# Kernel optimization log

Hardware: AMD Instinct MI355X
Metric: run time of the kernel (lower is better)

## Reference

```python
import jax, jax.numpy as jnp
import numpy as np

N, C, SI, VI, H, R = 10000, 2, 128, 16, 4, 32
SH, VH = SI // H, VI // H  # 32, 4
EPS = 1e-8

def _vnorm(x, axis):
    # clamped L2 norm, matches _norm_no_nan
    return jnp.sqrt(jnp.clip(jnp.sum(x * x, axis=axis), EPS, None))

def _gvp_full(s, v, wh, ws_w, ws_b, wv, wsv_w, wsv_b):
    # GVP with activations=(silu, sigmoid), vector_gate=True, vi=vo
    vh = jnp.swapaxes(v, -1, -2) @ wh            # [..., 3, h]
    vn = _vnorm(vh, -2)                          # [..., h]
    so = jnp.concatenate([s, vn], -1) @ ws_w + ws_b
    vo = jnp.swapaxes(vh @ wv, -1, -2)           # [..., vo, 3]
    gate = jax.nn.sigmoid(jax.nn.sigmoid(so) @ wsv_w + wsv_b)
    return jax.nn.silu(so), vo * gate[..., None]

def setup_inputs():
    key = jax.random.key(0)
    ks = iter(jax.random.split(key, 40))
    def lin(i, o):
        return jax.random.normal(next(ks), (i, o), jnp.float32) / np.sqrt(i)
    def bias(o):
        return 0.02 * jax.random.normal(next(ks), (o,), jnp.float32)
    inp = {}
    inp['s'] = jax.random.normal(next(ks), (N, C, SI), jnp.float32)
    inp['v'] = jax.random.normal(next(ks), (N, C, VI, 3), jnp.float32)
    # weight_proj: GVP((SI,VI)->(R,0)), no activations; h_dim = max(VI,0) = VI
    inp['wp_wh'] = lin(VI, VI); inp['wp_ws_w'] = lin(VI + SI, R); inp['wp_ws_b'] = bias(R)
    # to_q/k/v: GVP((SI,VI)->(SI,VI)), silu/sigmoid, vector_gate; h_dim = VI
    for p in ('q', 'k', 'vv'):
        inp[p + '_wh'] = lin(VI, VI)
        inp[p + '_ws_w'] = lin(VI + SI, SI); inp[p + '_ws_b'] = bias(SI)
        inp[p + '_wv'] = lin(VI, VI)
        inp[p + '_wsv_w'] = lin(SI, VI); inp[p + '_wsv_b'] = bias(VI)
    # attn_gvp_long: GVP((2*SH, 2*VH) -> (1,0)), no activations; h_dim = 2*VH
    inp['attn_wh'] = lin(2 * VH, 2 * VH)
    inp['attn_ws_w'] = lin(2 * VH + 2 * SH, 1); inp['attn_ws_b'] = bias(1)
    return inp

def reference(s, v, wp_wh, wp_ws_w, wp_ws_b,
              q_wh, q_ws_w, q_ws_b, q_wv, q_wsv_w, q_wsv_b,
              k_wh, k_ws_w, k_ws_b, k_wv, k_wsv_w, k_wsv_b,
              vv_wh, vv_ws_w, vv_ws_b, vv_wv, vv_wsv_w, vv_wsv_b,
              attn_wh, attn_ws_w, attn_ws_b):
    n, c = s.shape[:2]
    # ---- Compress: softmax-pool N -> R anchors ----
    vh = jnp.swapaxes(v, -1, -2) @ wp_wh          # [N,C,3,VI]
    vn = _vnorm(vh, -2)                            # [N,C,VI]
    pw = jnp.concatenate([s, vn], -1) @ wp_ws_w + wp_ws_b  # [N,C,R]
    pw = jax.nn.softmax(pw, axis=0)                # softmax over nodes
    s_g = jnp.einsum('nca,ncs->acs', pw, s)        # [R,C,SI] (includes transpose(0,1))
    v_g = jnp.einsum('nca,ncvd->acvd', pw, v)      # [R,C,VI,3]
    # ---- q from nodes, k/v from anchors ----
    qs, qv = _gvp_full(s, v, q_wh, q_ws_w, q_ws_b, q_wv, q_wsv_w, q_wsv_b)
    ks, kv = _gvp_full(s_g, v_g, k_wh, k_ws_w, k_ws_b, k_wv, k_wsv_w, k_wsv_b)
    vs, vv_ = _gvp_full(s_g, v_g, vv_wh, vv_ws_w, vv_ws_b, vv_wv, vv_wsv_w, vv_wsv_b)
    qs = qs.reshape(n, c, H, SH); qv = qv.reshape(n, c, H, VH, 3)
    ks = ks.reshape(R, c, H, SH); kv = kv.reshape(R, c, H, VH, 3)
    vs = vs.reshape(R, c, H, SH); vv_ = vv_.reshape(R, c, H, VH, 3)
    # ---- attention GVP on cat(q, k): split weights instead of materializing concat ----
    wh_q, wh_k = attn_wh[:VH], attn_wh[VH:]        # wh @ cat(qv,kv) = qv@wh_q + kv@wh_k
    qh = jnp.swapaxes(qv, -1, -2) @ wh_q           # [N,C,H,3,2VH]
    kh = jnp.swapaxes(kv, -1, -2) @ wh_k           # [R,C,H,3,2VH]
    vn2 = _vnorm(qh[:, None] + kh[None], -2)       # [N,R,C,H,2VH]
    ws_q = attn_ws_w[:SH]; ws_k = attn_ws_w[SH:2 * SH]; ws_n = attn_ws_w[2 * SH:]
    e = (qs @ ws_q)[:, None] + (ks @ ws_k)[None] + vn2 @ ws_n + attn_ws_b  # [N,R,C,H,1]
    e = e[..., 0] / np.sqrt(SH)
    alpha = jax.nn.softmax(e, axis=1)              # softmax over anchors (dim=1)
    # ---- Broadcast: weighted sum of anchor values ----
    out_s = jnp.einsum('nrch,rchd->nchd', alpha, vs).reshape(n, c, SI)
    out_v = jnp.einsum('nrch,rchde->nchde', alpha, vv_).reshape(n, c, VI, 3)
    return out_s, out_v
```

## Files before the change

kernel.cpp:

```cpp
#include <hip/hip_runtime.h>
#include <hip/hip_bf16.h>


#define N_  10000
#define C_  2
#define SI_ 128
#define VI_ 16
#define H_  4
#define R_  32
#define SH_ 32
#define VH_ 4
#define NC_ (N_*C_)

#define ROWS_ 16
#define XSTR_ 20

typedef const float* __restrict__ fptr;

__device__ __forceinline__ float sigm(float x){ return 1.f/(1.f+__expf(-x)); }

#define OFF_LG   0
#define OFF_EQH  640000
#define OFF_SG   2640000
#define OFF_TKH  2651520
#define OFF_TEK  2657664
#define OFF_TVS  2657920
#define OFF_TVV  2666112

#define SGSTRIDE_ 180

__global__ __launch_bounds__(256) void kA(
    fptr s, fptr v,
    fptr wp_wh, fptr wp_ws_w, fptr wp_ws_b,
    fptr q_wh, fptr q_ws_w, fptr q_ws_b, fptr q_wv, fptr q_wsv_w, fptr q_wsv_b,
    fptr attn_wh, fptr attn_ws_w,
    float* __restrict__ pexp, float* __restrict__ eqh,
    float* __restrict__ sgz)
{
  __shared__ __align__(16) float ARENA[160*XSTR_];
  __shared__ __align__(16) float VVs[ROWS_*48];
  __shared__ __align__(16) float VHQ[ROWS_*48];
  __shared__ __align__(16) float SO[ROWS_*128];
  __shared__ __align__(16) float GATE[ROWS_*16];
  __shared__ __align__(16) float QV[ROWS_*48];
  float* const XT  = ARENA;
  float* const SIG = ARENA;

  const int tid  = threadIdx.x;
  const int row0 = blockIdx.x * ROWS_;

  if (blockIdx.x == 0){
    for (int i = tid; i < 64*SGSTRIDE_; i += 256) sgz[i] = 0.f;
  }

  for (int idx = tid; idx < ROWS_*128; idx += 256){
    int r = idx >> 7, j = idx & 127;
    XT[j*XSTR_ + r] = s[(row0+r)*128 + j];
  }
  for (int idx = tid; idx < ROWS_*48; idx += 256){
    int r = idx / 48, k = idx - r*48;
    VVs[r*48 + k] = v[(row0+r)*48 + k];
  }
  __syncthreads();

  for (int idx = tid; idx < ROWS_*32; idx += 256){
    int r = idx >> 5, ii = idx & 31, path = ii >> 4, i = ii & 15;
    fptr wh = path ? wp_wh : q_wh;
    float h0=0.f, h1=0.f, h2=0.f;
    #pragma unroll
    for (int j = 0; j < 16; j++){
      float w = wh[j*16 + i];
      h0 = fmaf(VVs[r*48 + j*3 + 0], w, h0);
      h1 = fmaf(VVs[r*48 + j*3 + 1], w, h1);
      h2 = fmaf(VVs[r*48 + j*3 + 2], w, h2);
    }
    float vn = sqrtf(fmaxf(h0*h0 + h1*h1 + h2*h2, 1e-8f));
    if (!path){
      VHQ[r*48 +  0 + i] = h0;
      VHQ[r*48 + 16 + i] = h1;
      VHQ[r*48 + 32 + i] = h2;
      XT[(128+i)*XSTR_ + r] = vn;
    } else {
      XT[(144+i)*XSTR_ + r] = vn;
    }
  }
  __syncthreads();

  const int colA = tid & 127, rgA = tid >> 7;
  float acc[8];
  {
    float bqs = q_ws_b[colA];
    #pragma unroll
    for (int k = 0; k < 8; k++) acc[k] = bqs;
    const float* xbA = &XT[rgA*8];
    #pragma unroll 8
    for (int j = 0; j < 144; j++){
      float w = q_ws_w[j*128 + colA];
      const float* xb = xbA + j*XSTR_;
      float4 x0 = *(const float4*)(xb + 0);
      float4 x1 = *(const float4*)(xb + 4);
      acc[0] = fmaf(x0.x, w, acc[0]); acc[1] = fmaf(x0.y, w, acc[1]);
      acc[2] = fmaf(x0.z, w, acc[2]); acc[3] = fmaf(x0.w, w, acc[3]);
      acc[4] = fmaf(x1.x, w, acc[4]); acc[5] = fmaf(x1.y, w, acc[5]);
      acc[6] = fmaf(x1.z, w, acc[6]); acc[7] = fmaf(x1.w, w, acc[7]);
    }
  }
  {
    const int colB = tid & 31, rgB = tid >> 5;
    float b0 = wp_ws_b[colB];
    float a0 = b0, a1 = b0;
    #pragma unroll 8
    for (int j = 0; j < 144; j++){
      int jj = (j < 128) ? j : (j + 16);
      float w = wp_ws_w[j*32 + colB];
      const float* xb = &XT[jj*XSTR_ + rgB*2];
      a0 = fmaf(xb[0], w, a0);
      a1 = fmaf(xb[1], w, a1);
    }
    const int n = (row0 >> 1) + rgB;
    pexp[(0*32 + colB)*N_ + n] = __expf(a0);
    pexp[(1*32 + colB)*N_ + n] = __expf(a1);
  }
  __syncthreads();

  #pragma unroll
  for (int k = 0; k < 8; k++){
    float so = acc[k];
    float sg_ = sigm(so);
    SIG[(rgA*8 + k)*128 + colA] = sg_;
    SO [(rgA*8 + k)*128 + colA] = so * sg_;
  }
  __syncthreads();

  {
    const int r = tid >> 4, g = tid & 15;
    float ga = q_wsv_b[g];
    #pragma unroll 8
    for (int o = 0; o < 128; o += 4){
      float4 s4 = *(const float4*)&SIG[r*128 + o];
      ga = fmaf(s4.x, q_wsv_w[(o+0)*16 + g], ga);
      ga = fmaf(s4.y, q_wsv_w[(o+1)*16 + g], ga);
      ga = fmaf(s4.z, q_wsv_w[(o+2)*16 + g], ga);
      ga = fmaf(s4.w, q_wsv_w[(o+3)*16 + g], ga);
    }
    GATE[r*16 + g] = sigm(ga);
  }
  __syncthreads();

  for (int t = tid; t < 64 + ROWS_*48; t += 256){
    if (t < 64){
      const int r = t >> 2, h = t & 3;
      float e = 0.f;
      #pragma unroll
      for (int u = 0; u < 32; u++)
        e = fmaf(SO[r*128 + h*32 + u], attn_ws_w[u], e);
      eqh[(row0 + r)*100 + h] = e;
    } else {
      const int t2 = t - 64;
      int r = t2 / 48, k = t2 - r*48, i = k / 3, d = k - i*3;
      float a = 0.f;
      #pragma unroll
      for (int j = 0; j < 16; j++)
        a = fmaf(VHQ[r*48 + d*16 + j], q_wv[j*16 + i], a);
      QV[r*48 + k] = a * GATE[r*16 + i];
    }
  }
  __syncthreads();

  for (int t = tid; t < ROWS_*96; t += 256){
    int r = t / 96, k = t - r*96;
    int h = k / 24, rem = k - h*24, d = rem >> 3, ee = rem & 7;
    float a = 0.f;
    #pragma unroll
    for (int i = 0; i < 4; i++)
      a = fmaf(QV[r*48 + (h*4 + i)*3 + d], attn_wh[i*8 + ee], a);
    eqh[(row0 + r)*100 + 8 + k] = a;
  }
}

__global__ __launch_bounds__(256) void kAccum(const float* __restrict__ pexp,
                                              fptr s, fptr v,
                                              float* __restrict__ sg)
{
  const int b = blockIdx.x;
  const int c = b & 1, ah = (b >> 1) & 1, chunk = b >> 2;
  const int n0 = chunk * 50;
  const int tid = threadIdx.x;
  const int ag = tid >> 6, dl = tid & 63;
  const int abase = ah*16 + ag*4;

  const float* pb = pexp + (c*32 + abase)*N_;
  float acc[4][3] = {};
  float dn[4] = {};

  #pragma unroll 2
  for (int n = n0; n < n0 + 50; n++){
    const int rc = n*2 + c;
    float pw[4];
    #pragma unroll
    for (int aa = 0; aa < 4; aa++){
      pw[aa] = pb[aa*N_ + n];
      dn[aa] += pw[aa];
    }
    #pragma unroll
    for (int dd = 0; dd < 3; dd++){
      int d = dl + 64*dd;
      if (d < 176){
        float xv = (d < 128) ? s[rc*128 + d] : v[rc*48 + d - 128];
        #pragma unroll
        for (int aa = 0; aa < 4; aa++)
          acc[aa][dd] = fmaf(pw[aa], xv, acc[aa][dd]);
      }
    }
  }
  #pragma unroll
  for (int aa = 0; aa < 4; aa++){
    const int base = (c*32 + abase + aa)*SGSTRIDE_;
    #pragma unroll
    for (int dd = 0; dd < 3; dd++){
      int d = dl + 64*dd;
      if (d < 176) atomicAdd(&sg[base + d], acc[aa][dd]);
    }
    if (dl == 0) atomicAdd(&sg[base + 176], dn[aa]);
  }
}

__global__ __launch_bounds__(256) void kSmall(
    const float* __restrict__ sg,
    fptr k_wh, fptr k_ws_w, fptr k_ws_b, fptr k_wv, fptr k_wsv_w, fptr k_wsv_b,
    fptr vv_wh, fptr vv_ws_w, fptr vv_ws_b, fptr vv_wv, fptr vv_wsv_w, fptr vv_wsv_b,
    fptr attn_wh, fptr attn_ws_w,
    float* __restrict__ tkh, float* __restrict__ tek,
    float* __restrict__ tvs, float* __restrict__ tvv)
{
  const int b = blockIdx.x, r = b >> 1, c = b & 1;
  const int tid = threadIdx.x;
  __shared__ float X[176];
  __shared__ float VN[2][16];
  __shared__ float VH[2][48];
  __shared__ float SOk[128], SOv[128];
  __shared__ float G[2][16];
  __shared__ float KV[48];

  if (tid < 176){
    const float* p = sg + (c*32 + r)*SGSTRIDE_;
    X[tid] = p[tid] / p[176];
  }
  __syncthreads();

  if (tid < 32){
    int path = tid >> 4, i = tid & 15;
    fptr wh = path ? vv_wh : k_wh;
    float h0=0.f, h1=0.f, h2=0.f;
    #pragma unroll
    for (int j = 0; j < 16; j++){
      float w = wh[j*16 + i];
      h0 = fmaf(X[128 + j*3 + 0], w, h0);
      h1 = fmaf(X[128 + j*3 + 1], w, h1);
      h2 = fmaf(X[128 + j*3 + 2], w, h2);
    }
    VH[path][ 0 + i] = h0; VH[path][16 + i] = h1; VH[path][32 + i] = h2;
    VN[path][i] = sqrtf(fmaxf(h0*h0 + h1*h1 + h2*h2, 1e-8f));
  }
  __syncthreads();

  {
    int path = tid >> 7, col = tid & 127;
    fptr W  = path ? vv_ws_w : k_ws_w;
    fptr Bb = path ? vv_ws_b : k_ws_b;
    float so = Bb[col];
    for (int j = 0; j < 128; j++) so = fmaf(X[j], W[j*128 + col], so);
    #pragma unroll
    for (int i = 0; i < 16; i++)  so = fmaf(VN[path][i], W[(128+i)*128 + col], so);
    (path ? SOv : SOk)[col] = so;
  }
  __syncthreads();

  if (tid < 32){
    int path = tid >> 4, g = tid & 15;
    fptr Wsv = path ? vv_wsv_w : k_wsv_w;
    fptr Bsv = path ? vv_wsv_b : k_wsv_b;
    const float* SOp = path ? SOv : SOk;
    float ga = Bsv[g];
    for (int o = 0; o < 128; o++)
      ga = fmaf(sigm(SOp[o]), Wsv[o*16 + g], ga);
    G[path][g] = sigm(ga);
  } else if (tid < 36){
    int h = tid - 32;
    float e = 0.f;
    #pragma unroll
    for (int t = 0; t < 32; t++){
      float so = SOk[h*32 + t];
      e = fmaf(so * sigm(so), attn_ws_w[32 + t], e);
    }
    tek[(r*2 + c)*4 + h] = e;
  } else if (tid >= 64 && tid < 192){
    int o = tid - 64;
    float so = SOv[o];
    tvs[(r*2 + c)*128 + o] = so * sigm(so);
  }
  __syncthreads();

  if (tid < 96){
    int path = tid / 48, k = tid % 48, i = k / 3, d = k - i*3;
    fptr Wv = path ? vv_wv : k_wv;
    float vo = 0.f;
    #pragma unroll
    for (int j = 0; j < 16; j++)
      vo = fmaf(VH[path][d*16 + j], Wv[j*16 + i], vo);
    float gv = vo * G[path][i];
    if (path == 0) KV[k] = gv;
    else {
      int h = i >> 2, ii = i & 3;
      tvv[(((r*2 + c)*4 + h)*4 + ii)*3 + d] = gv;
    }
  }
  __syncthreads();

  if (tid < 96){
    int h = tid / 24, rem = tid % 24, d = rem >> 3, ee = rem & 7;
    float a = 0.f;
    #pragma unroll
    for (int i = 0; i < 4; i++)
      a = fmaf(KV[(h*4 + i)*3 + d], attn_wh[(4 + i)*8 + ee], a);
    tkh[((r*2 + c)*4 + h)*24 + d*8 + ee] = a;
  }
}

__global__ __launch_bounds__(256) void kAttn(
    const float* __restrict__ eqh,
    const float* __restrict__ tkh, const float* __restrict__ tek,
    const float* __restrict__ tvs, const float* __restrict__ tvv,
    fptr attn_ws_w, fptr attn_ws_b,
    float* __restrict__ out)
{
  __shared__ __align__(16) float KH[64*28];
  __shared__ __align__(16) float VS[64*36];
  __shared__ __align__(16) float VV[64*12];
  __shared__ float EK[64];
  const int tid = threadIdx.x;
  const int h      = blockIdx.x & 3;
  const int rowblk = blockIdx.x >> 2;

  for (int i = tid; i < 64*24; i += 256){
    int m = i / 24, t = i - m*24;
    KH[m*28 + t] = tkh[(m*4 + h)*24 + t];
  }
  for (int i = tid; i < 64*32; i += 256){
    int m = i >> 5, t = i & 31;
    VS[m*36 + t] = tvs[m*128 + h*32 + t];
  }
  for (int i = tid; i < 64*12; i += 256){
    int m = i / 12, t = i - m*12;
    VV[m*12 + t] = tvv[(m*4 + h)*12 + t];
  }
  if (tid < 64) EK[tid] = tek[tid*4 + h];

  float wsn[8];
  #pragma unroll
  for (int ee = 0; ee < 8; ee++) wsn[ee] = attn_ws_w[64 + ee];
  const float wb = attn_ws_b[0];
  __syncthreads();

  const int rh  = tid & 3;
  const int row = rowblk*64 + (tid >> 2);
  if (row < NC_){
    const int c = row & 1;
    const float eq = eqh[row*100 + h];
    float qh[24];
    {
      const float4* qp = (const float4*)&eqh[row*100 + 8 + h*24];
      #pragma unroll
      for (int k = 0; k < 6; k++){
        float4 t4 = qp[k];
        qh[k*4+0] = t4.x; qh[k*4+1] = t4.y; qh[k*4+2] = t4.z; qh[k*4+3] = t4.w;
      }
    }
    float4 accs4[8];
    float4 accv4[3];
    #pragma unroll
    for (int q = 0; q < 8; q++) accs4[q] = make_float4(0.f,0.f,0.f,0.f);
    #pragma unroll
    for (int q = 0; q < 3; q++) accv4[q] = make_float4(0.f,0.f,0.f,0.f);
    float den = 0.f;

    #pragma unroll
    for (int rr = 0; rr < 8; rr++){
      const int m = (rh*8 + rr)*2 + c;
      const float* khp = &KH[m*28];
      float en = 0.f;
      #pragma unroll
      for (int ee = 0; ee < 8; ee++){
        float a0 = qh[ee]      + khp[ee];
        float a1 = qh[8 + ee]  + khp[8 + ee];
        float a2 = qh[16 + ee] + khp[16 + ee];
        en = fmaf(sqrtf(fmaxf(a0*a0 + a1*a1 + a2*a2, 1e-8f)), wsn[ee], en);
      }
      const float w = __expf((eq + EK[m] + en + wb) * 0.17677669529663687f);
      den += w;
      const float4* vp4 = (const float4*)&VS[m*36];
      #pragma unroll
      for (int q = 0; q < 8; q++){
        float4 t4 = vp4[q];
        accs4[q].x = fmaf(w, t4.x, accs4[q].x);
        accs4[q].y = fmaf(w, t4.y, accs4[q].y);
        accs4[q].z = fmaf(w, t4.z, accs4[q].z);
        accs4[q].w = fmaf(w, t4.w, accs4[q].w);
      }
      const float4* vv4 = (const float4*)&VV[m*12];
      #pragma unroll
      for (int q = 0; q < 3; q++){
        float4 t4 = vv4[q];
        accv4[q].x = fmaf(w, t4.x, accv4[q].x);
        accv4[q].y = fmaf(w, t4.y, accv4[q].y);
        accv4[q].z = fmaf(w, t4.z, accv4[q].z);
        accv4[q].w = fmaf(w, t4.w, accv4[q].w);
      }
    }

    #pragma unroll
    for (int q = 0; q < 8; q++){
      accs4[q].x += __shfl_xor(accs4[q].x, 1, 64);
      accs4[q].x += __shfl_xor(accs4[q].x, 2, 64);
      accs4[q].y += __shfl_xor(accs4[q].y, 1, 64);
      accs4[q].y += __shfl_xor(accs4[q].y, 2, 64);
      accs4[q].z += __shfl_xor(accs4[q].z, 1, 64);
      accs4[q].z += __shfl_xor(accs4[q].z, 2, 64);
      accs4[q].w += __shfl_xor(accs4[q].w, 1, 64);
      accs4[q].w += __shfl_xor(accs4[q].w, 2, 64);
    }
    #pragma unroll
    for (int q = 0; q < 3; q++){
      accv4[q].x += __shfl_xor(accv4[q].x, 1, 64);
      accv4[q].x += __shfl_xor(accv4[q].x, 2, 64);
      accv4[q].y += __shfl_xor(accv4[q].y, 1, 64);
      accv4[q].y += __shfl_xor(accv4[q].y, 2, 64);
      accv4[q].z += __shfl_xor(accv4[q].z, 1, 64);
      accv4[q].z += __shfl_xor(accv4[q].z, 2, 64);
      accv4[q].w += __shfl_xor(accv4[q].w, 1, 64);
      accv4[q].w += __shfl_xor(accv4[q].w, 2, 64);
    }
    den += __shfl_xor(den, 1, 64);
    den += __shfl_xor(den, 2, 64);

    if (rh == 0){
      const float inv = 1.f / den;
      float4* po = (float4*)&out[row*128 + h*32];
      #pragma unroll
      for (int q = 0; q < 8; q++){
        float4 t4 = accs4[q];
        t4.x *= inv; t4.y *= inv; t4.z *= inv; t4.w *= inv;
        po[q] = t4;
      }
      float4* pv = (float4*)&out[NC_*128 + row*48 + h*12];
      #pragma unroll
      for (int q = 0; q < 3; q++){
        float4 t4 = accv4[q];
        t4.x *= inv; t4.y *= inv; t4.z *= inv; t4.w *= inv;
        pv[q] = t4;
      }
    }
  }
}

extern "C" void kernel_launch(void* const* d_in, const int* in_sizes, int n_in,
                              void* d_out, int out_size, void* d_ws, size_t ws_size,
                              hipStream_t stream)
{
  fptr s        = (fptr)d_in[0];
  fptr v        = (fptr)d_in[1];
  fptr wp_wh    = (fptr)d_in[2];
  fptr wp_ws_w  = (fptr)d_in[3];
  fptr wp_ws_b  = (fptr)d_in[4];
  fptr q_wh     = (fptr)d_in[5];
  fptr q_ws_w   = (fptr)d_in[6];
  fptr q_ws_b   = (fptr)d_in[7];
  fptr q_wv     = (fptr)d_in[8];
  fptr q_wsv_w  = (fptr)d_in[9];
  fptr q_wsv_b  = (fptr)d_in[10];
  fptr k_wh     = (fptr)d_in[11];
  fptr k_ws_w   = (fptr)d_in[12];
  fptr k_ws_b   = (fptr)d_in[13];
  fptr k_wv     = (fptr)d_in[14];
  fptr k_wsv_w  = (fptr)d_in[15];
  fptr k_wsv_b  = (fptr)d_in[16];
  fptr vv_wh    = (fptr)d_in[17];
  fptr vv_ws_w  = (fptr)d_in[18];
  fptr vv_ws_b  = (fptr)d_in[19];
  fptr vv_wv    = (fptr)d_in[20];
  fptr vv_wsv_w = (fptr)d_in[21];
  fptr vv_wsv_b = (fptr)d_in[22];
  fptr attn_wh  = (fptr)d_in[23];
  fptr attn_ws_w= (fptr)d_in[24];
  fptr attn_ws_b= (fptr)d_in[25];

  float* ws   = (float*)d_ws;
  float* pexp = ws + OFF_LG;
  float* eqh  = ws + OFF_EQH;
  float* sg   = ws + OFF_SG;
  float* tkh  = ws + OFF_TKH;
  float* tek  = ws + OFF_TEK;
  float* tvs  = ws + OFF_TVS;
  float* tvv  = ws + OFF_TVV;

  kA<<<NC_/ROWS_, 256, 0, stream>>>(s, v, wp_wh, wp_ws_w, wp_ws_b,
                                    q_wh, q_ws_w, q_ws_b, q_wv, q_wsv_w, q_wsv_b,
                                    attn_wh, attn_ws_w, pexp, eqh, sg);
  kAccum<<<800, 256, 0, stream>>>(pexp, s, v, sg);
  kSmall<<<64, 256, 0, stream>>>(sg,
                                 k_wh, k_ws_w, k_ws_b, k_wv, k_wsv_w, k_wsv_b,
                                 vv_wh, vv_ws_w, vv_ws_b, vv_wv, vv_wsv_w, vv_wsv_b,
                                 attn_wh, attn_ws_w, tkh, tek, tvs, tvv);
  kAttn<<<((NC_ + 63)/64)*4, 256, 0, stream>>>(eqh, tkh, tek, tvs, tvv,
                                               attn_ws_w, attn_ws_b, (float*)d_out);
}
```

Before: 232.8 us.

## Restructure kA projection GEMM to row-per-lane with fused wp path and attention dot

```diff
diff --git a/kernel.cpp b/kernel.cpp
--- a/kernel.cpp
+++ b/kernel.cpp
@@ -13,7 +13,9 @@
 #define NC_ (N_*C_)
 
 #define ROWS_ 16
-#define XSTR_ 20
+#define XR_   132
+#define VNR_  18
+#define SGR_  129
 
 typedef const float* __restrict__ fptr;
 
@@ -37,14 +39,14 @@
     float* __restrict__ pexp, float* __restrict__ eqh,
     float* __restrict__ sgz)
 {
-  __shared__ __align__(16) float ARENA[160*XSTR_];
+  __shared__ __align__(16) float X[16*XR_];
+  __shared__ float VNQ[16*VNR_];
+  __shared__ float VNP[16*VNR_];
   __shared__ __align__(16) float VVs[ROWS_*48];
   __shared__ __align__(16) float VHQ[ROWS_*48];
-  __shared__ __align__(16) float SO[ROWS_*128];
+  __shared__ float SIG[16*SGR_];
   __shared__ __align__(16) float GATE[ROWS_*16];
   __shared__ __align__(16) float QV[ROWS_*48];
-  float* const XT  = ARENA;
-  float* const SIG = ARENA;
 
   const int tid  = threadIdx.x;
   const int row0 = blockIdx.x * ROWS_;
@@ -55,7 +57,7 @@
 
   for (int idx = tid; idx < ROWS_*128; idx += 256){
     int r = idx >> 7, j = idx & 127;
-    XT[j*XSTR_ + r] = s[(row0+r)*128 + j];
+    X[r*XR_ + j] = s[(row0+r)*128 + j];
   }
   for (int idx = tid; idx < ROWS_*48; idx += 256){
     int r = idx / 48, k = idx - r*48;
@@ -79,102 +81,135 @@
       VHQ[r*48 +  0 + i] = h0;
       VHQ[r*48 + 16 + i] = h1;
       VHQ[r*48 + 32 + i] = h2;
-      XT[(128+i)*XSTR_ + r] = vn;
+      VNQ[r*VNR_ + i] = vn;
     } else {
-      XT[(144+i)*XSTR_ + r] = vn;
-    }
-  }
-  __syncthreads();
-
-  const int colA = tid & 127, rgA = tid >> 7;
+      VNP[r*VNR_ + i] = vn;
+    }
+  }
+  __syncthreads();
+
+  const int r  = tid & 15;
+  const int cg = tid >> 4;
+  const float* xrow = &X[r*XR_];
+  fptr wqb = q_ws_w  + cg*8;
+  fptr wpb = wp_ws_w + cg*2;
+
   float acc[8];
+  #pragma unroll
+  for (int cc = 0; cc < 8; cc++) acc[cc] = q_ws_b[cg*8 + cc];
+  float b2[2];
+  b2[0] = wp_ws_b[cg*2]; b2[1] = wp_ws_b[cg*2 + 1];
+
+  #pragma unroll 2
+  for (int j4 = 0; j4 < 32; j4++){
+    const int j = j4*4;
+    float4 x4 = *(const float4*)(xrow + j);
+    {
+      float4 wa = *(const float4*)(wqb + (j+0)*128);
+      float4 wb = *(const float4*)(wqb + (j+0)*128 + 4);
+      float2 wp = *(const float2*)(wpb + (j+0)*32);
+      acc[0]=fmaf(x4.x,wa.x,acc[0]); acc[1]=fmaf(x4.x,wa.y,acc[1]);
+      acc[2]=fmaf(x4.x,wa.z,acc[2]); acc[3]=fmaf(x4.x,wa.w,acc[3]);
+      acc[4]=fmaf(x4.x,wb.x,acc[4]); acc[5]=fmaf(x4.x,wb.y,acc[5]);
+      acc[6]=fmaf(x4.x,wb.z,acc[6]); acc[7]=fmaf(x4.x,wb.w,acc[7]);
+      b2[0]=fmaf(x4.x,wp.x,b2[0]);   b2[1]=fmaf(x4.x,wp.y,b2[1]);
+    }
+    {
+      float4 wa = *(const float4*)(wqb + (j+1)*128);
+      float4 wb = *(const float4*)(wqb + (j+1)*128 + 4);
+      float2 wp = *(const float2*)(wpb + (j+1)*32);
+      acc[0]=fmaf(x4.y,wa.x,acc[0]); acc[1]=fmaf(x4.y,wa.y,acc[1]);
+      acc[2]=fmaf(x4.y,wa.z,acc[2]); acc[3]=fmaf(x4.y,wa.w,acc[3]);
+      acc[4]=fmaf(x4.y,wb.x,acc[4]); acc[5]=fmaf(x4.y,wb.y,acc[5]);
+      acc[6]=fmaf(x4.y,wb.z,acc[6]); acc[7]=fmaf(x4.y,wb.w,acc[7]);
+      b2[0]=fmaf(x4.y,wp.x,b2[0]);   b2[1]=fmaf(x4.y,wp.y,b2[1]);
+    }
+    {
+      float4 wa = *(const float4*)(wqb + (j+2)*128);
+      float4 wb = *(const float4*)(wqb + (j+2)*128 + 4);
+      float2 wp = *(const float2*)(wpb + (j+2)*32);
+      acc[0]=fmaf(x4.z,wa.x,acc[0]); acc[1]=fmaf(x4.z,wa.y,acc[1]);
+      acc[2]=fmaf(x4.z,wa.z,acc[2]); acc[3]=fmaf(x4.z,wa.w,acc[3]);
+      acc[4]=fmaf(x4.z,wb.x,acc[4]); acc[5]=fmaf(x4.z,wb.y,acc[5]);
+      acc[6]=fmaf(x4.z,wb.z,acc[6]); acc[7]=fmaf(x4.z,wb.w,acc[7]);
+      b2[0]=fmaf(x4.z,wp.x,b2[0]);   b2[1]=fmaf(x4.z,wp.y,b2[1]);
+    }
+    {
+      float4 wa = *(const float4*)(wqb + (j+3)*128);
+      float4 wb = *(const float4*)(wqb + (j+3)*128 + 4);
+      float2 wp = *(const float2*)(wpb + (j+3)*32);
+      acc[0]=fmaf(x4.w,wa.x,acc[0]); acc[1]=fmaf(x4.w,wa.y,acc[1]);
+      acc[2]=fmaf(x4.w,wa.z,acc[2]); acc[3]=fmaf(x4.w,wa.w,acc[3]);
+      acc[4]=fmaf(x4.w,wb.x,acc[4]); acc[5]=fmaf(x4.w,wb.y,acc[5]);
+      acc[6]=fmaf(x4.w,wb.z,acc[6]); acc[7]=fmaf(x4.w,wb.w,acc[7]);
+      b2[0]=fmaf(x4.w,wp.x,b2[0]);   b2[1]=fmaf(x4.w,wp.y,b2[1]);
+    }
+  }
+  #pragma unroll 4
+  for (int i = 0; i < 16; i++){
+    float xq = VNQ[r*VNR_ + i];
+    float4 wa = *(const float4*)(wqb + (128+i)*128);
+    float4 wb = *(const float4*)(wqb + (128+i)*128 + 4);
+    acc[0]=fmaf(xq,wa.x,acc[0]); acc[1]=fmaf(xq,wa.y,acc[1]);
+    acc[2]=fmaf(xq,wa.z,acc[2]); acc[3]=fmaf(xq,wa.w,acc[3]);
+    acc[4]=fmaf(xq,wb.x,acc[4]); acc[5]=fmaf(xq,wb.y,acc[5]);
+    acc[6]=fmaf(xq,wb.z,acc[6]); acc[7]=fmaf(xq,wb.w,acc[7]);
+    float xp = VNP[r*VNR_ + i];
+    float2 wp = *(const float2*)(wpb + (128+i)*32);
+    b2[0]=fmaf(xp,wp.x,b2[0]);   b2[1]=fmaf(xp,wp.y,b2[1]);
+  }
+
   {
-    float bqs = q_ws_b[colA];
-    #pragma unroll
-    for (int k = 0; k < 8; k++) acc[k] = bqs;
-    const float* xbA = &XT[rgA*8];
-    #pragma unroll 8
-    for (int j = 0; j < 144; j++){
-      float w = q_ws_w[j*128 + colA];
-      const float* xb = xbA + j*XSTR_;
-      float4 x0 = *(const float4*)(xb + 0);
-      float4 x1 = *(const float4*)(xb + 4);
-      acc[0] = fmaf(x0.x, w, acc[0]); acc[1] = fmaf(x0.y, w, acc[1]);
-      acc[2] = fmaf(x0.z, w, acc[2]); acc[3] = fmaf(x0.w, w, acc[3]);
-      acc[4] = fmaf(x1.x, w, acc[4]); acc[5] = fmaf(x1.y, w, acc[5]);
-      acc[6] = fmaf(x1.z, w, acc[6]); acc[7] = fmaf(x1.w, w, acc[7]);
-    }
+    float ep = 0.f;
+    const int tq = (cg & 3)*8;
+    #pragma unroll
+    for (int cc = 0; cc < 8; cc++){
+      float so  = acc[cc];
+      float sg_ = sigm(so);
+      SIG[r*SGR_ + cg*8 + cc] = sg_;
+      ep = fmaf(so*sg_, attn_ws_w[tq + cc], ep);
+    }
+    ep += __shfl_xor(ep, 16, 64);
+    ep += __shfl_xor(ep, 32, 64);
+    if ((tid & 63) < 16)
+      eqh[(row0 + r)*100 + (cg >> 2)] = ep;
   }
   {
-    const int colB = tid & 31, rgB = tid >> 5;
-    float b0 = wp_ws_b[colB];
-    float a0 = b0, a1 = b0;
-    #pragma unroll 8
-    for (int j = 0; j < 144; j++){
-      int jj = (j < 128) ? j : (j + 16);
-      float w = wp_ws_w[j*32 + colB];
-      const float* xb = &XT[jj*XSTR_ + rgB*2];
-      a0 = fmaf(xb[0], w, a0);
-      a1 = fmaf(xb[1], w, a1);
-    }
-    const int n = (row0 >> 1) + rgB;
-    pexp[(0*32 + colB)*N_ + n] = __expf(a0);
-    pexp[(1*32 + colB)*N_ + n] = __expf(a1);
-  }
-  __syncthreads();
-
-  #pragma unroll
-  for (int k = 0; k < 8; k++){
-    float so = acc[k];
-    float sg_ = sigm(so);
-    SIG[(rgA*8 + k)*128 + colA] = sg_;
-    SO [(rgA*8 + k)*128 + colA] = so * sg_;
+    const int gr = row0 + r, c = gr & 1, n = gr >> 1;
+    pexp[(c*32 + cg*2    )*N_ + n] = __expf(b2[0]);
+    pexp[(c*32 + cg*2 + 1)*N_ + n] = __expf(b2[1]);
   }
   __syncthreads();
 
   {
-    const int r = tid >> 4, g = tid & 15;
+    const int rr = tid >> 4, g = tid & 15;
+    const float* sp = &SIG[rr*SGR_];
     float ga = q_wsv_b[g];
     #pragma unroll 8
-    for (int o = 0; o < 128; o += 4){
-      float4 s4 = *(const float4*)&SIG[r*128 + o];
-      ga = fmaf(s4.x, q_wsv_w[(o+0)*16 + g], ga);
-      ga = fmaf(s4.y, q_wsv_w[(o+1)*16 + g], ga);
-      ga = fmaf(s4.z, q_wsv_w[(o+2)*16 + g], ga);
-      ga = fmaf(s4.w, q_wsv_w[(o+3)*16 + g], ga);
-    }
-    GATE[r*16 + g] = sigm(ga);
-  }
-  __syncthreads();
-
-  for (int t = tid; t < 64 + ROWS_*48; t += 256){
-    if (t < 64){
-      const int r = t >> 2, h = t & 3;
-      float e = 0.f;
-      #pragma unroll
-      for (int u = 0; u < 32; u++)
-        e = fmaf(SO[r*128 + h*32 + u], attn_ws_w[u], e);
-      eqh[(row0 + r)*100 + h] = e;
-    } else {
-      const int t2 = t - 64;
-      int r = t2 / 48, k = t2 - r*48, i = k / 3, d = k - i*3;
-      float a = 0.f;
-      #pragma unroll
-      for (int j = 0; j < 16; j++)
-        a = fmaf(VHQ[r*48 + d*16 + j], q_wv[j*16 + i], a);
-      QV[r*48 + k] = a * GATE[r*16 + i];
-    }
+    for (int o = 0; o < 128; o++)
+      ga = fmaf(sp[o], q_wsv_w[o*16 + g], ga);
+    GATE[rr*16 + g] = sigm(ga);
+  }
+  __syncthreads();
+
+  for (int t = tid; t < ROWS_*48; t += 256){
+    int rr = t / 48, k = t - rr*48, i = k / 3, d = k - i*3;
+    float a = 0.f;
+    #pragma unroll
+    for (int j = 0; j < 16; j++)
+      a = fmaf(VHQ[rr*48 + d*16 + j], q_wv[j*16 + i], a);
+    QV[rr*48 + k] = a * GATE[rr*16 + i];
   }
   __syncthreads();
 
   for (int t = tid; t < ROWS_*96; t += 256){
-    int r = t / 96, k = t - r*96;
+    int rr = t / 96, k = t - rr*96;
     int h = k / 24, rem = k - h*24, d = rem >> 3, ee = rem & 7;
     float a = 0.f;
     #pragma unroll
     for (int i = 0; i < 4; i++)
-      a = fmaf(QV[r*48 + (h*4 + i)*3 + d], attn_wh[i*8 + ee], a);
-    eqh[(row0 + r)*100 + 8 + k] = a;
+      a = fmaf(QV[rr*48 + (h*4 + i)*3 + d], attn_wh[i*8 + ee], a);
+    eqh[(row0 + rr)*100 + 8 + k] = a;
   }
 }
 
```

Measured after the change: 269.7 us. 15.9% more time.
